# Optimization experiments

Hardware: AMD Instinct MI355X
Metric: run time of the kernel (lower is better)

The kernel has to match this reference:

```python
import jax, jax.numpy as jnp
import numpy as np

B, T, C = 2, 2048, 1024
H = 16
D = C // H
STRIDE = 2
EPS = 1e-5


def _strided_allowed(T, stride):
    # position i attends to j if j<=i and (j >= i-4 local band OR j % stride == 0)
    i = jnp.arange(T)[:, None]
    j = jnp.arange(T)[None, :]
    return (j <= i) & ((j >= i - 4) | (j % stride == 0))


def _layernorm(x, w, b):
    mu = jnp.mean(x, axis=-1, keepdims=True)
    var = jnp.mean(jnp.square(x - mu), axis=-1, keepdims=True)
    return (x - mu) * jax.lax.rsqrt(var + EPS) * w + b


def setup_inputs() -> dict:
    key = jax.random.key(0)
    ks = jax.random.split(key, 8)
    s = 0.02
    return {
        "x": jax.random.normal(ks[0], (B, T, C), dtype=jnp.float32),
        "ln1_w": jnp.ones((C,), jnp.float32),
        "ln1_b": jnp.zeros((C,), jnp.float32),
        "c_attn_w": s * jax.random.normal(ks[1], (C, 3 * C), jnp.float32),  # [in,out]
        "c_attn_b": jnp.zeros((3 * C,), jnp.float32),
        "attn_proj_w": s * jax.random.normal(ks[2], (C, C), jnp.float32),
        "attn_proj_b": jnp.zeros((C,), jnp.float32),
        "ln2_w": jnp.ones((C,), jnp.float32),
        "ln2_b": jnp.zeros((C,), jnp.float32),
        "fc_w": s * jax.random.normal(ks[3], (C, 4 * C), jnp.float32),
        "fc_b": jnp.zeros((4 * C,), jnp.float32),
        "mlp_proj_w": s * jax.random.normal(ks[4], (4 * C, C), jnp.float32),
        "mlp_proj_b": jnp.zeros((C,), jnp.float32),
    }


def reference(x, ln1_w, ln1_b, c_attn_w, c_attn_b, attn_proj_w, attn_proj_b,
              ln2_w, ln2_b, fc_w, fc_b, mlp_proj_w, mlp_proj_b):
    Bx, Tx, Cx = x.shape
    # --- sparse (strided) causal attention on ln_1(x) ---
    h = _layernorm(x, ln1_w, ln1_b)
    qkv = h @ c_attn_w + c_attn_b                      # [B,T,3C]
    q, k, v = jnp.split(qkv, 3, axis=-1)
    q = q.reshape(Bx, Tx, H, D).transpose(0, 2, 1, 3)  # [B,H,T,D]
    k = k.reshape(Bx, Tx, H, D).transpose(0, 2, 1, 3)
    v = v.reshape(Bx, Tx, H, D).transpose(0, 2, 1, 3)
    scale = 1.0 / np.sqrt(D)
    att = jnp.einsum('bhqd,bhkd->bhqk', q, k) * scale  # dense [B,H,T,T] as in source
    allowed = _strided_allowed(Tx, STRIDE)             # [T,T] bool
    att = jnp.where(allowed[None, None], att, -jnp.inf)
    att = jax.nn.softmax(att, axis=-1)
    y = jnp.einsum('bhqk,bhkd->bhqd', att, v)
    y = y.transpose(0, 2, 1, 3).reshape(Bx, Tx, Cx)
    y = y @ attn_proj_w + attn_proj_b
    x = x + y
    # --- MLP on ln_2(x) ---
    h2 = _layernorm(x, ln2_w, ln2_b)
    h2 = jax.nn.gelu(h2 @ fc_w + fc_b, approximate=False)
    x = x + (h2 @ mlp_proj_w + mlp_proj_b)
    return x
```

## Files before the change

### kernel.cpp

```cpp
#include <hip/hip_runtime.h>
#include <hip/hip_bf16.h>

#define Bn 2
#define Tn 2048
#define Cn 1024
#define Hn 16
#define Dn 64
#define Mrows (Bn * Tn)

typedef __attribute__((ext_vector_type(8))) short short8;
typedef __attribute__((ext_vector_type(4))) float f32x4;

typedef const __attribute__((address_space(1))) unsigned int* gas_ptr;
typedef __attribute__((address_space(3))) unsigned int* las_ptr;

__device__ __forceinline__ unsigned short f2b(float f) {
  unsigned int u = __builtin_bit_cast(unsigned int, f);
  return (unsigned short)((u + 0x7fffu + ((u >> 16) & 1u)) >> 16);
}

__device__ __forceinline__ float gelu_f(float v) {
  float u2 = v + 0.044715f * v * v * v;
  float e = __expf(1.5957691216f * u2);
  float th = 1.0f - 2.0f / (e + 1.0f);
  return 0.5f * v * (1.0f + th);
}

__global__ __launch_bounds__(256) void ln_kernel(const float* __restrict__ x,
                                                 const float* __restrict__ w,
                                                 const float* __restrict__ b,
                                                 unsigned short* __restrict__ out) {
  const int row = blockIdx.x;
  const int t = threadIdx.x;
  const float4 v = *reinterpret_cast<const float4*>(x + (size_t)row * Cn + t * 4);
  float s = v.x + v.y + v.z + v.w;
  float s2 = v.x * v.x + v.y * v.y + v.z * v.z + v.w * v.w;
#pragma unroll
  for (int m = 1; m < 64; m <<= 1) { s += __shfl_xor(s, m); s2 += __shfl_xor(s2, m); }
  __shared__ float ls[4], ls2[4];
  if ((t & 63) == 0) { ls[t >> 6] = s; ls2[t >> 6] = s2; }
  __syncthreads();
  s  = ls[0] + ls[1] + ls[2] + ls[3];
  s2 = ls2[0] + ls2[1] + ls2[2] + ls2[3];
  const float mu = s * (1.0f / Cn);
  const float rstd = rsqrtf(s2 * (1.0f / Cn) - mu * mu + 1e-5f);
  const float4 wv = *reinterpret_cast<const float4*>(w + t * 4);
  const float4 bv = *reinterpret_cast<const float4*>(b + t * 4);
  unsigned short o[4];
  o[0] = f2b((v.x - mu) * rstd * wv.x + bv.x);
  o[1] = f2b((v.y - mu) * rstd * wv.y + bv.y);
  o[2] = f2b((v.z - mu) * rstd * wv.z + bv.z);
  o[3] = f2b((v.w - mu) * rstd * wv.w + bv.w);
  *reinterpret_cast<uint2*>(out + (size_t)row * Cn + t * 4) = *reinterpret_cast<uint2*>(o);
}

__global__ __launch_bounds__(256) void transpose_bf16_kernel(const float* __restrict__ W,
                                                             unsigned short* __restrict__ Wt,
                                                             int K, int N) {
  __shared__ float tile[32][33];
  const int n0 = blockIdx.x * 32, k0 = blockIdx.y * 32;
  const int tx = threadIdx.x & 31, ty = threadIdx.x >> 5;
#pragma unroll
  for (int r = 0; r < 4; r++)
    tile[ty + r * 8][tx] = W[(size_t)(k0 + ty + r * 8) * N + n0 + tx];
  __syncthreads();
#pragma unroll
  for (int r = 0; r < 4; r++)
    Wt[(size_t)(n0 + ty + r * 8) * K + k0 + tx] = f2b(tile[tx][ty + r * 8]);
}

#define BUFS 16384
template <int EP>
__global__ __launch_bounds__(512, 2) void gemm256_kernel(
    const unsigned short* __restrict__ A, const unsigned short* __restrict__ Bt,
    const float* __restrict__ bias, void* out, int M, int N, int K, int nx) {
  extern __shared__ unsigned short lds[];
  const int tid = threadIdx.x;
  const int lane = tid & 63, w = tid >> 6;
  const int wm = w >> 2, wn = w & 3;
  const int l15 = lane & 15, l4 = lane >> 4;

  const int nwg = gridDim.x;
  int wg = blockIdx.x;
  wg = (wg & 7) * (nwg >> 3) + (wg >> 3);
  const int tile_m = (wg / nx) * 256;
  const int tile_n = (wg % nx) * 256;

  f32x4 acc[8][4] = {};

  const int ch0 = w * 64 + lane;
  const int r0 = ch0 >> 2;
  const int c0 = (((ch0 & 3) ^ ((r0 >> 1) & 3))) * 8;
  const unsigned short* gA0 = A + (size_t)(tile_m + r0) * K + c0;
  const unsigned short* gA1 = gA0 + (size_t)128 * K;
  const unsigned short* gB0 = Bt + (size_t)(tile_n + r0) * K + c0;
  const unsigned short* gB1 = gB0 + (size_t)128 * K;
  const int ldsA0 = (w * 64) * 8, ldsA1 = (512 + w * 64) * 8;

  auto stage = [&](unsigned short* Ab, int t) {
    unsigned short* Bb = Ab + 8192;
    const size_t ko = (size_t)t * 32;
    __builtin_amdgcn_global_load_lds((gas_ptr)(gA0 + ko), (las_ptr)&Ab[ldsA0], 16, 0, 0);
    __builtin_amdgcn_global_load_lds((gas_ptr)(gA1 + ko), (las_ptr)&Ab[ldsA1], 16, 0, 0);
    __builtin_amdgcn_global_load_lds((gas_ptr)(gB0 + ko), (las_ptr)&Bb[ldsA0], 16, 0, 0);
    __builtin_amdgcn_global_load_lds((gas_ptr)(gB1 + ko), (las_ptr)&Bb[ldsA1], 16, 0, 0);
  };

  stage(lds, 0);
  stage(lds + BUFS, 1);
  stage(lds + 2 * BUFS, 2);
  asm volatile("s_waitcnt vmcnt(8)" ::: "memory");
  __builtin_amdgcn_s_barrier();
  __builtin_amdgcn_sched_barrier(0);

  const int ca = (l4 ^ ((l15 >> 1) & 3)) * 8;

  const int nt = K >> 5;
  for (int tb = 0; tb < nt; tb += 4) {
#pragma unroll
    for (int u = 0; u < 4; u++) {
      const int t = tb + u;
      if (t + 3 < nt) stage(lds + (((u + 3) & 3) * BUFS), t + 3);

      const unsigned short* Ab = lds + u * BUFS;
      const unsigned short* Bb = Ab + 8192;
      short8 a[4], b[4], a2[4];
#pragma unroll
      for (int i = 0; i < 4; i++) {
        a[i] = *reinterpret_cast<const short8*>(&Ab[(wm * 128 + i * 16 + l15) * 32 + ca]);
        b[i] = *reinterpret_cast<const short8*>(&Bb[(wn * 64 + i * 16 + l15) * 32 + ca]);
      }
      __builtin_amdgcn_sched_barrier(0);
#pragma unroll
      for (int i = 0; i < 4; i++)
        a2[i] = *reinterpret_cast<const short8*>(&Ab[(wm * 128 + 64 + i * 16 + l15) * 32 + ca]);

      asm volatile("s_waitcnt lgkmcnt(4)" ::: "memory");
      __builtin_amdgcn_sched_barrier(0);
      __builtin_amdgcn_s_setprio(1);
#pragma unroll
      for (int mi = 0; mi < 4; mi++)
#pragma unroll
        for (int ni = 0; ni < 4; ni++)
          acc[mi][ni] = __builtin_amdgcn_mfma_f32_16x16x32_bf16(a[mi], b[ni], acc[mi][ni], 0, 0, 0);
      __builtin_amdgcn_s_setprio(0);
      __builtin_amdgcn_sched_barrier(0);

      asm volatile("s_waitcnt lgkmcnt(0)" ::: "memory");
      __builtin_amdgcn_sched_barrier(0);
      __builtin_amdgcn_s_setprio(1);
#pragma unroll
      for (int mi = 0; mi < 4; mi++)
#pragma unroll
        for (int ni = 0; ni < 4; ni++)
          acc[mi + 4][ni] = __builtin_amdgcn_mfma_f32_16x16x32_bf16(a2[mi], b[ni], acc[mi + 4][ni], 0, 0, 0);
      __builtin_amdgcn_s_setprio(0);
      __builtin_amdgcn_sched_barrier(0);

      if (t + 3 < nt) {
        asm volatile("s_waitcnt vmcnt(8)" ::: "memory");
      } else if (t + 2 < nt) {
        asm volatile("s_waitcnt vmcnt(4)" ::: "memory");
      } else if (t + 1 < nt) {
        asm volatile("s_waitcnt vmcnt(0)" ::: "memory");
      }
      __builtin_amdgcn_s_barrier();
      __builtin_amdgcn_sched_barrier(0);
    }
  }

#pragma unroll
  for (int ni = 0; ni < 4; ni++) {
    const int col = tile_n + wn * 64 + ni * 16 + l15;
    const float bv = bias[col];
#pragma unroll
    for (int mi = 0; mi < 8; mi++) {
#pragma unroll
      for (int r = 0; r < 4; r++) {
        const int row = tile_m + wm * 128 + mi * 16 + l4 * 4 + r;
        const size_t idx = (size_t)row * N + col;
        float v = acc[mi][ni][r] + bv;
        if (EP == 0) {
          ((unsigned short*)out)[idx] = f2b(v);
        } else {
          ((unsigned short*)out)[idx] = f2b(gelu_f(v));
        }
      }
    }
  }
}

__global__ __launch_bounds__(512, 2) void gemm128_kernel(
    const unsigned short* __restrict__ A, const unsigned short* __restrict__ Bt,
    const float* __restrict__ bias, const float* __restrict__ res, float* __restrict__ out,
    int M, int N, int K, int nx) {
  extern __shared__ unsigned short lds[];
  const int tid = threadIdx.x;
  const int lane = tid & 63, w = tid >> 6;
  const int wm = w >> 2, wn = w & 3;
  const int l15 = lane & 15, l4 = lane >> 4;

  const int nwg = gridDim.x;
  int wg = blockIdx.x;
  wg = (wg & 7) * (nwg >> 3) + (wg >> 3);
  const int tile_m = (wg / nx) * 128;
  const int tile_n = (wg % nx) * 128;

  f32x4 acc[4][2] = {};

  const unsigned short* Gs = (w < 4) ? A : Bt;
  const int tb0 = (w < 4) ? tile_m : tile_n;
  const int ch0 = (w & 3) * 128 + lane;
  const int r0c = ch0 >> 2;
  const int c0s = (((ch0 & 3) ^ ((r0c >> 1) & 3))) * 8;
  const unsigned short* g0 = Gs + (size_t)(tb0 + r0c) * K + c0s;
  const unsigned short* g1 = g0 + (size_t)16 * K;
  const int lds0 = ((w & 3) * 128) * 8, lds1 = ((w & 3) * 128 + 64) * 8;
  const int half = (w < 4) ? 0 : 4096;

  auto stage = [&](unsigned short* slot, int t) {
    unsigned short* Lb = slot + half;
    const size_t ko = (size_t)t * 32;
    __builtin_amdgcn_global_load_lds((gas_ptr)(g0 + ko), (las_ptr)&Lb[lds0], 16, 0, 0);
    __builtin_amdgcn_global_load_lds((gas_ptr)(g1 + ko), (las_ptr)&Lb[lds1], 16, 0, 0);
  };

  stage(lds, 0);
  stage(lds + 8192, 1);
  stage(lds + 16384, 2);
  asm volatile("s_waitcnt vmcnt(4)" ::: "memory");
  __builtin_amdgcn_s_barrier();
  __builtin_amdgcn_sched_barrier(0);

  const int ca = (l4 ^ ((l15 >> 1) & 3)) * 8;

  const int nt = K >> 5;
  for (int tb = 0; tb < nt; tb += 4) {
#pragma unroll
    for (int u = 0; u < 4; u++) {
      const int t = tb + u;
      if (t + 3 < nt) stage(lds + ((u + 3) & 3) * 8192, t + 3);

      const unsigned short* Ab = lds + u * 8192;
      const unsigned short* Bb = Ab + 4096;
      short8 a[2], b[2], a2[2];
#pragma unroll
      for (int i = 0; i < 2; i++) {
        a[i] = *reinterpret_cast<const short8*>(&Ab[(wm * 64 + i * 16 + l15) * 32 + ca]);
        b[i] = *reinterpret_cast<const short8*>(&Bb[(wn * 32 + i * 16 + l15) * 32 + ca]);
      }
      __builtin_amdgcn_sched_barrier(0);
#pragma unroll
      for (int i = 0; i < 2; i++)
        a2[i] = *reinterpret_cast<const short8*>(&Ab[(wm * 64 + 32 + i * 16 + l15) * 32 + ca]);

      asm volatile("s_waitcnt lgkmcnt(2)" ::: "memory");
      __builtin_amdgcn_sched_barrier(0);
      __builtin_amdgcn_s_setprio(1);
#pragma unroll
      for (int mi = 0; mi < 2; mi++)
#pragma unroll
        for (int ni = 0; ni < 2; ni++)
          acc[mi][ni] = __builtin_amdgcn_mfma_f32_16x16x32_bf16(a[mi], b[ni], acc[mi][ni], 0, 0, 0);
      __builtin_amdgcn_s_setprio(0);
      __builtin_amdgcn_sched_barrier(0);

      asm volatile("s_waitcnt lgkmcnt(0)" ::: "memory");
      __builtin_amdgcn_sched_barrier(0);
      __builtin_amdgcn_s_setprio(1);
#pragma unroll
      for (int mi = 0; mi < 2; mi++)
#pragma unroll
        for (int ni = 0; ni < 2; ni++)
          acc[mi + 2][ni] = __builtin_amdgcn_mfma_f32_16x16x32_bf16(a2[mi], b[ni], acc[mi + 2][ni], 0, 0, 0);
      __builtin_amdgcn_s_setprio(0);
      __builtin_amdgcn_sched_barrier(0);

      if (t + 3 < nt) {
        asm volatile("s_waitcnt vmcnt(4)" ::: "memory");
      } else if (t + 2 < nt) {
        asm volatile("s_waitcnt vmcnt(2)" ::: "memory");
      } else if (t + 1 < nt) {
        asm volatile("s_waitcnt vmcnt(0)" ::: "memory");
      }
      __builtin_amdgcn_s_barrier();
      __builtin_amdgcn_sched_barrier(0);
    }
  }

#pragma unroll
  for (int ni = 0; ni < 2; ni++) {
    const int col = tile_n + wn * 32 + ni * 16 + l15;
    const float bv = bias[col];
#pragma unroll
    for (int mi = 0; mi < 4; mi++) {
#pragma unroll
      for (int r = 0; r < 4; r++) {
        const int row = tile_m + wm * 64 + mi * 16 + l4 * 4 + r;
        const size_t idx = (size_t)row * N + col;
        out[idx] = acc[mi][ni][r] + bv + res[idx];
      }
    }
  }
}

__global__ __launch_bounds__(256, 4) void attn_kernel(const unsigned short* __restrict__ qkv,
                                                      unsigned short* __restrict__ y) {
  __shared__ unsigned short SH[17408];
  const int tid = threadIdx.x;
  const int lane = tid & 63, w = tid >> 6;
  const int l15 = lane & 15, l4 = lane >> 4;

  const int bi = blockIdx.x;
  const int quarter = bi >> 8, rest = bi & 255;
  const int bh = rest >> 3, sub = rest & 7;
  int qt;
  if (quarter == 0) qt = sub;
  else if (quarter == 1) qt = 15 - sub;
  else if (quarter == 2) qt = 16 + sub;
  else qt = 31 - sub;
  const int bb = bh >> 4, hh = bh & 15;
  const int q0 = qt * 64;
  const size_t base = (size_t)bb * Tn * (3 * Cn) + hh * 64;

  const int nfar = qt >> 1;
  const int ntiles = nfar + (q0 ? 2 : 1);

  unsigned short* Vt = SH + 8192;
  unsigned short* Ps = SH + 12800 + w * 1152;

  auto keyof = [&](int t, int row) -> int {
    if (t < nfar) return t * 128 + 2 * row;
    return q0 - 64 * (ntiles - 1 - t) + row;
  };
  auto stageK = [&](int t) {
    unsigned short* kb = SH + ((t & 1) << 12);
#pragma unroll
    for (int u = 0; u < 2; u++) {
      const int chunk = u * 256 + tid;
      const int row = chunk >> 3, cc = chunk & 7;
      const int csrc = cc ^ (row & 7);
      const int key = keyof(t, row);
      __builtin_amdgcn_global_load_lds(
          (gas_ptr)&qkv[base + Cn + (size_t)key * (3 * Cn) + csrc * 8],
          (las_ptr)&kb[(u * 256 + (w << 6)) * 8], 16, 0, 0);
    }
  };
  uint4 vr[2];
  auto fetchV = [&](int t) {
#pragma unroll
    for (int u = 0; u < 2; u++) {
      const int chunk = u * 256 + tid;
      const int row = chunk >> 3, cc = chunk & 7;
      const int key = keyof(t, row);
      vr[u] = *reinterpret_cast<const uint4*>(&qkv[base + 2 * Cn + (size_t)key * (3 * Cn) + cc * 8]);
    }
  };

#pragma unroll
  for (int u = 0; u < 2; u++) {
    const int chunk = u * 256 + tid;
    const int row = chunk >> 3, cc = chunk & 7;
    const int csrc = cc ^ (row & 7);
    __builtin_amdgcn_global_load_lds(
        (gas_ptr)&qkv[base + (size_t)(q0 + row) * (3 * Cn) + csrc * 8],
        (las_ptr)&SH[(u * 256 + (w << 6)) * 8], 16, 0, 0);
  }
  __syncthreads();
  short8 qf[2];
#pragma unroll
  for (int ks = 0; ks < 2; ks++) {
    const int r = (w << 4) + l15;
    qf[ks] = *reinterpret_cast<const short8*>(&SH[r * 64 + (((ks * 4 + l4) ^ (l15 & 7)) * 8)]);
  }
  asm volatile("s_waitcnt lgkmcnt(0)" ::: "memory");
  __builtin_amdgcn_s_barrier();
  __builtin_amdgcn_sched_barrier(0);
  stageK(0);
  fetchV(0);
  __syncthreads();

  f32x4 acc_o[4] = {};
  float mrow[4], lrow[4];
#pragma unroll
  for (int r = 0; r < 4; r++) { mrow[r] = -1e30f; lrow[r] = 0.0f; }

  for (int t = 0; t < ntiles; ++t) {
#pragma unroll
    for (int u = 0; u < 2; u++) {
      const int chunk = u * 256 + tid;
      const int row = chunk >> 3, cc = chunk & 7;
      unsigned short tmp[8];
      *reinterpret_cast<uint4*>(tmp) = vr[u];
      const int xr = row ^ (cc << 3);
#pragma unroll
      for (int j = 0; j < 8; j++) Vt[(cc * 8 + j) * 72 + xr] = tmp[j];
    }
    if (t + 1 < ntiles) { stageK(t + 1); fetchV(t + 1); }
    asm volatile("s_waitcnt lgkmcnt(0)" ::: "memory");
    __builtin_amdgcn_s_barrier();
    __builtin_amdgcn_sched_barrier(0);

    const unsigned short* Kb = SH + ((t & 1) << 12);
    f32x4 s[4] = {};
#pragma unroll
    for (int ni = 0; ni < 4; ni++) {
#pragma unroll
      for (int ks = 0; ks < 2; ks++) {
        const int r = ni * 16 + l15;
        short8 kf = *reinterpret_cast<const short8*>(&Kb[r * 64 + (((ks * 4 + l4) ^ (l15 & 7)) * 8)]);
        s[ni] = __builtin_amdgcn_mfma_f32_16x16x32_bf16(qf[ks], kf, s[ni], 0, 0, 0);
      }
    }

    const bool far = (t < nfar);
    const int kb0 = far ? t * 128 : q0 - 64 * (ntiles - 1 - t);
#pragma unroll
    for (int ni = 0; ni < 4; ni++) {
      const int pos = ni * 16 + l15;
      const int j = far ? kb0 + 2 * pos : kb0 + pos;
#pragma unroll
      for (int r = 0; r < 4; r++) {
        float v = s[ni][r] * 0.125f;
        if (far) {
          v = (j < q0 - 64) ? v : -1e30f;
        } else {
          const int iq = q0 + (w << 4) + l4 * 4 + r;
          const bool ok = (j <= iq) && ((j >= iq - 4) || ((j & 1) == 0));
          v = ok ? v : -1e30f;
        }
        s[ni][r] = v;
      }
    }

#pragma unroll
    for (int r = 0; r < 4; r++) {
      float tm = fmaxf(fmaxf(s[0][r], s[1][r]), fmaxf(s[2][r], s[3][r]));
      tm = fmaxf(tm, __shfl_xor(tm, 1));
      tm = fmaxf(tm, __shfl_xor(tm, 2));
      tm = fmaxf(tm, __shfl_xor(tm, 4));
      tm = fmaxf(tm, __shfl_xor(tm, 8));
      const float mnew = fmaxf(mrow[r], tm);
      const float alpha = __expf(mrow[r] - mnew);
      mrow[r] = mnew;
      lrow[r] *= alpha;
#pragma unroll
      for (int nd = 0; nd < 4; nd++) acc_o[nd][r] *= alpha;
      float rs = 0.0f;
#pragma unroll
      for (int ni = 0; ni < 4; ni++) {
        const float pv = __expf(s[ni][r] - mnew);
        s[ni][r] = pv;
        rs += pv;
      }
      rs += __shfl_xor(rs, 1); rs += __shfl_xor(rs, 2);
      rs += __shfl_xor(rs, 4); rs += __shfl_xor(rs, 8);
      lrow[r] += rs;
    }

#pragma unroll
    for (int ni = 0; ni < 4; ni++)
#pragma unroll
      for (int r = 0; r < 4; r++)
        Ps[(l4 * 4 + r) * 72 + ni * 16 + l15] = f2b(s[ni][r]);

#pragma unroll
    for (int kss = 0; kss < 2; kss++) {
      short8 pf = *reinterpret_cast<const short8*>(&Ps[l15 * 72 + kss * 32 + l4 * 8]);
#pragma unroll
      for (int nd = 0; nd < 4; nd++) {
        const int d = nd * 16 + l15;
        const int kcol = (kss * 32 + l4 * 8) ^ ((d >> 3) << 3);
        short8 vf = *reinterpret_cast<const short8*>(&Vt[d * 72 + kcol]);
        acc_o[nd] = __builtin_amdgcn_mfma_f32_16x16x32_bf16(pf, vf, acc_o[nd], 0, 0, 0);
      }
    }

    __syncthreads();
  }

#pragma unroll
  for (int r = 0; r < 4; r++) {
    const float inv = 1.0f / lrow[r];
    const int row = q0 + (w << 4) + l4 * 4 + r;
#pragma unroll
    for (int nd = 0; nd < 4; nd++) {
      const int col = nd * 16 + l15;
      y[((size_t)bb * Tn + row) * Cn + hh * 64 + col] = f2b(acc_o[nd][r] * inv);
    }
  }
}

extern "C" void kernel_launch(void* const* d_in, const int* in_sizes, int n_in,
                              void* d_out, int out_size, void* d_ws, size_t ws_size,
                              hipStream_t stream) {
  const float* x           = (const float*)d_in[0];
  const float* ln1_w       = (const float*)d_in[1];
  const float* ln1_b       = (const float*)d_in[2];
  const float* c_attn_w    = (const float*)d_in[3];
  const float* c_attn_b    = (const float*)d_in[4];
  const float* attn_proj_w = (const float*)d_in[5];
  const float* attn_proj_b = (const float*)d_in[6];
  const float* ln2_w       = (const float*)d_in[7];
  const float* ln2_b       = (const float*)d_in[8];
  const float* fc_w        = (const float*)d_in[9];
  const float* fc_b        = (const float*)d_in[10];
  const float* mlp_proj_w  = (const float*)d_in[11];
  const float* mlp_proj_b  = (const float*)d_in[12];
  float* out = (float*)d_out;

  char* ws = (char*)d_ws;
  unsigned short* wT1 = (unsigned short*)(ws);
  unsigned short* wT2 = (unsigned short*)(ws + 6291456);
  unsigned short* wT3 = (unsigned short*)(ws + 8388608);
  unsigned short* wT4 = (unsigned short*)(ws + 16777216);
  unsigned short* h   = (unsigned short*)(ws + 25165824);
  unsigned short* qkv = (unsigned short*)(ws + 33554432);
  unsigned short* yb  = (unsigned short*)(ws + 67108864);

  hipFuncSetAttribute((const void*)gemm256_kernel<0>, hipFuncAttributeMaxDynamicSharedMemorySize, 131072);
  hipFuncSetAttribute((const void*)gemm256_kernel<2>, hipFuncAttributeMaxDynamicSharedMemorySize, 131072);
  hipFuncSetAttribute((const void*)gemm128_kernel, hipFuncAttributeMaxDynamicSharedMemorySize, 65536);

  transpose_bf16_kernel<<<dim3(3072 / 32, 1024 / 32), 256, 0, stream>>>(c_attn_w, wT1, 1024, 3072);
  transpose_bf16_kernel<<<dim3(1024 / 32, 1024 / 32), 256, 0, stream>>>(attn_proj_w, wT2, 1024, 1024);
  transpose_bf16_kernel<<<dim3(4096 / 32, 1024 / 32), 256, 0, stream>>>(fc_w, wT3, 1024, 4096);
  transpose_bf16_kernel<<<dim3(1024 / 32, 4096 / 32), 256, 0, stream>>>(mlp_proj_w, wT4, 4096, 1024);

  ln_kernel<<<Mrows, 256, 0, stream>>>(x, ln1_w, ln1_b, h);
  gemm256_kernel<0><<<(Mrows / 256) * (3072 / 256), 512, 131072, stream>>>(
      h, wT1, c_attn_b, qkv, Mrows, 3072, 1024, 3072 / 256);
  attn_kernel<<<1024, 256, 0, stream>>>(qkv, yb);
  gemm128_kernel<<<(Mrows / 128) * (1024 / 128), 512, 65536, stream>>>(
      yb, wT2, attn_proj_b, x, out, Mrows, 1024, 1024, 1024 / 128);
  ln_kernel<<<Mrows, 256, 0, stream>>>(out, ln2_w, ln2_b, h);
  gemm256_kernel<2><<<(Mrows / 256) * (4096 / 256), 512, 131072, stream>>>(
      h, wT3, fc_b, qkv, Mrows, 4096, 1024, 4096 / 256);
  gemm128_kernel<<<(Mrows / 128) * (1024 / 128), 512, 65536, stream>>>(
      qkv, wT4, mlp_proj_b, out, out, Mrows, 1024, 4096, 1024 / 128);
}
```

Measured before the change: 228.7 us.

## Fuse weight prep with LN1, deepen gemm128 pipeline, lazily rescale softmax

Merges the four weight transpose launches and the first layernorm into one prep kernel to cut launch overhead and tail gaps. Rewrites the gemm128 main loop to process two K-steps per iteration with a six-slot LDS ring and a prefetch distance of four, raising its shared memory to 96KB and launch bounds to one block per CU. In attention, the online-softmax rescale now runs only when some row maximum grows by more than 8, skipping exp/multiply work at the cost of possibly larger unnormalized values. The lower occupancy in gemm128 may offset its deeper prefetch.

New measurement: 221.4 us. 3.2% less time.

```diff
diff --git a/kernel.cpp b/kernel.cpp
--- a/kernel.cpp
+++ b/kernel.cpp
@@ -26,18 +26,15 @@
   return 0.5f * v * (1.0f + th);
 }
 
-__global__ __launch_bounds__(256) void ln_kernel(const float* __restrict__ x,
-                                                 const float* __restrict__ w,
-                                                 const float* __restrict__ b,
-                                                 unsigned short* __restrict__ out) {
-  const int row = blockIdx.x;
+__device__ __forceinline__ void ln_row(const float* __restrict__ x, const float* __restrict__ w,
+                                       const float* __restrict__ b, unsigned short* __restrict__ out,
+                                       int row, float* ls, float* ls2) {
   const int t = threadIdx.x;
   const float4 v = *reinterpret_cast<const float4*>(x + (size_t)row * Cn + t * 4);
   float s = v.x + v.y + v.z + v.w;
   float s2 = v.x * v.x + v.y * v.y + v.z * v.z + v.w * v.w;
 #pragma unroll
   for (int m = 1; m < 64; m <<= 1) { s += __shfl_xor(s, m); s2 += __shfl_xor(s2, m); }
-  __shared__ float ls[4], ls2[4];
   if ((t & 63) == 0) { ls[t >> 6] = s; ls2[t >> 6] = s2; }
   __syncthreads();
   s  = ls[0] + ls[1] + ls[2] + ls[3];
@@ -54,11 +51,35 @@
   *reinterpret_cast<uint2*>(out + (size_t)row * Cn + t * 4) = *reinterpret_cast<uint2*>(o);
 }
 
-__global__ __launch_bounds__(256) void transpose_bf16_kernel(const float* __restrict__ W,
-                                                             unsigned short* __restrict__ Wt,
-                                                             int K, int N) {
+__global__ __launch_bounds__(256) void ln_kernel(const float* __restrict__ x,
+                                                 const float* __restrict__ w,
+                                                 const float* __restrict__ b,
+                                                 unsigned short* __restrict__ out) {
+  __shared__ float ls[4], ls2[4];
+  ln_row(x, w, b, out, blockIdx.x, ls, ls2);
+}
+
+__global__ __launch_bounds__(256) void prep_kernel(
+    const float* __restrict__ W0, unsigned short* __restrict__ T0,
+    const float* __restrict__ W1, unsigned short* __restrict__ T1,
+    const float* __restrict__ W2, unsigned short* __restrict__ T2,
+    const float* __restrict__ W3, unsigned short* __restrict__ T3,
+    const float* __restrict__ x, const float* __restrict__ ln1w,
+    const float* __restrict__ ln1b, unsigned short* __restrict__ h) {
   __shared__ float tile[32][33];
-  const int n0 = blockIdx.x * 32, k0 = blockIdx.y * 32;
+  __shared__ float ls[4], ls2[4];
+  int b = blockIdx.x;
+  if (b >= 12288) {
+    ln_row(x, ln1w, ln1b, h, b - 12288, ls, ls2);
+    return;
+  }
+  const float* W; unsigned short* T; int K, N;
+  if (b < 3072)      { W = W0; T = T0; K = 1024; N = 3072; }
+  else if (b < 4096) { W = W1; T = T1; K = 1024; N = 1024; b -= 3072; }
+  else if (b < 8192) { W = W2; T = T2; K = 1024; N = 4096; b -= 4096; }
+  else               { W = W3; T = T3; K = 4096; N = 1024; b -= 8192; }
+  const int nx = N >> 5;
+  const int n0 = (b % nx) * 32, k0 = (b / nx) * 32;
   const int tx = threadIdx.x & 31, ty = threadIdx.x >> 5;
 #pragma unroll
   for (int r = 0; r < 4; r++)
@@ -66,7 +87,7 @@
   __syncthreads();
 #pragma unroll
   for (int r = 0; r < 4; r++)
-    Wt[(size_t)(n0 + ty + r * 8) * K + k0 + tx] = f2b(tile[tx][ty + r * 8]);
+    T[(size_t)(n0 + ty + r * 8) * K + k0 + tx] = f2b(tile[tx][ty + r * 8]);
 }
 
 #define BUFS 16384
@@ -190,7 +211,7 @@
   }
 }
 
-__global__ __launch_bounds__(512, 2) void gemm128_kernel(
+__global__ __launch_bounds__(512, 1) void gemm128_kernel(
     const unsigned short* __restrict__ A, const unsigned short* __restrict__ Bt,
     const float* __restrict__ bias, const float* __restrict__ res, float* __restrict__ out,
     int M, int N, int K, int nx) {
@@ -218,16 +239,17 @@
   const int lds0 = ((w & 3) * 128) * 8, lds1 = ((w & 3) * 128 + 64) * 8;
   const int half = (w < 4) ? 0 : 4096;
 
-  auto stage = [&](unsigned short* slot, int t) {
-    unsigned short* Lb = slot + half;
+  auto stage = [&](int slot, int t) {
+    unsigned short* Lb = lds + slot * 8192 + half;
     const size_t ko = (size_t)t * 32;
     __builtin_amdgcn_global_load_lds((gas_ptr)(g0 + ko), (las_ptr)&Lb[lds0], 16, 0, 0);
     __builtin_amdgcn_global_load_lds((gas_ptr)(g1 + ko), (las_ptr)&Lb[lds1], 16, 0, 0);
   };
 
-  stage(lds, 0);
-  stage(lds + 8192, 1);
-  stage(lds + 16384, 2);
+  stage(0, 0);
+  stage(1, 1);
+  stage(2, 2);
+  stage(3, 3);
   asm volatile("s_waitcnt vmcnt(4)" ::: "memory");
   __builtin_amdgcn_s_barrier();
   __builtin_amdgcn_sched_barrier(0);
@@ -235,57 +257,88 @@
   const int ca = (l4 ^ ((l15 >> 1) & 3)) * 8;
 
   const int nt = K >> 5;
-  for (int tb = 0; tb < nt; tb += 4) {
-#pragma unroll
-    for (int u = 0; u < 4; u++) {
-      const int t = tb + u;
-      if (t + 3 < nt) stage(lds + ((u + 3) & 3) * 8192, t + 3);
-
-      const unsigned short* Ab = lds + u * 8192;
-      const unsigned short* Bb = Ab + 4096;
-      short8 a[2], b[2], a2[2];
-#pragma unroll
-      for (int i = 0; i < 2; i++) {
-        a[i] = *reinterpret_cast<const short8*>(&Ab[(wm * 64 + i * 16 + l15) * 32 + ca]);
-        b[i] = *reinterpret_cast<const short8*>(&Bb[(wn * 32 + i * 16 + l15) * 32 + ca]);
-      }
-      __builtin_amdgcn_sched_barrier(0);
-#pragma unroll
-      for (int i = 0; i < 2; i++)
-        a2[i] = *reinterpret_cast<const short8*>(&Ab[(wm * 64 + 32 + i * 16 + l15) * 32 + ca]);
-
-      asm volatile("s_waitcnt lgkmcnt(2)" ::: "memory");
-      __builtin_amdgcn_sched_barrier(0);
-      __builtin_amdgcn_s_setprio(1);
-#pragma unroll
-      for (int mi = 0; mi < 2; mi++)
-#pragma unroll
-        for (int ni = 0; ni < 2; ni++)
-          acc[mi][ni] = __builtin_amdgcn_mfma_f32_16x16x32_bf16(a[mi], b[ni], acc[mi][ni], 0, 0, 0);
-      __builtin_amdgcn_s_setprio(0);
-      __builtin_amdgcn_sched_barrier(0);
-
-      asm volatile("s_waitcnt lgkmcnt(0)" ::: "memory");
-      __builtin_amdgcn_sched_barrier(0);
-      __builtin_amdgcn_s_setprio(1);
-#pragma unroll
-      for (int mi = 0; mi < 2; mi++)
-#pragma unroll
-        for (int ni = 0; ni < 2; ni++)
-          acc[mi + 2][ni] = __builtin_amdgcn_mfma_f32_16x16x32_bf16(a2[mi], b[ni], acc[mi + 2][ni], 0, 0, 0);
-      __builtin_amdgcn_s_setprio(0);
-      __builtin_amdgcn_sched_barrier(0);
-
-      if (t + 3 < nt) {
-        asm volatile("s_waitcnt vmcnt(4)" ::: "memory");
-      } else if (t + 2 < nt) {
-        asm volatile("s_waitcnt vmcnt(2)" ::: "memory");
-      } else if (t + 1 < nt) {
-        asm volatile("s_waitcnt vmcnt(0)" ::: "memory");
-      }
-      __builtin_amdgcn_s_barrier();
-      __builtin_amdgcn_sched_barrier(0);
-    }
+  const int np = nt >> 1;
+  for (int p = 0; p < np; ++p) {
+    const int t0 = 2 * p;
+    if (t0 + 4 < nt) stage((t0 + 4) % 6, t0 + 4);
+    if (t0 + 5 < nt) stage((t0 + 5) % 6, t0 + 5);
+
+    const unsigned short* A0 = lds + (t0 % 6) * 8192;
+    const unsigned short* B0 = A0 + 4096;
+    const unsigned short* A1 = lds + ((t0 + 1) % 6) * 8192;
+    const unsigned short* B1 = A1 + 4096;
+    short8 a[2], b[2], a2[2], c[2], d[2], c2[2];
+#pragma unroll
+    for (int i = 0; i < 2; i++) {
+      a[i] = *reinterpret_cast<const short8*>(&A0[(wm * 64 + i * 16 + l15) * 32 + ca]);
+      b[i] = *reinterpret_cast<const short8*>(&B0[(wn * 32 + i * 16 + l15) * 32 + ca]);
+    }
+    __builtin_amdgcn_sched_barrier(0);
+#pragma unroll
+    for (int i = 0; i < 2; i++)
+      a2[i] = *reinterpret_cast<const short8*>(&A0[(wm * 64 + 32 + i * 16 + l15) * 32 + ca]);
+    __builtin_amdgcn_sched_barrier(0);
+#pragma unroll
+    for (int i = 0; i < 2; i++) {
+      c[i] = *reinterpret_cast<const short8*>(&A1[(wm * 64 + i * 16 + l15) * 32 + ca]);
+      d[i] = *reinterpret_cast<const short8*>(&B1[(wn * 32 + i * 16 + l15) * 32 + ca]);
+    }
+    __builtin_amdgcn_sched_barrier(0);
+#pragma unroll
+    for (int i = 0; i < 2; i++)
+      c2[i] = *reinterpret_cast<const short8*>(&A1[(wm * 64 + 32 + i * 16 + l15) * 32 + ca]);
+
+    asm volatile("s_waitcnt lgkmcnt(8)" ::: "memory");
+    __builtin_amdgcn_sched_barrier(0);
+    __builtin_amdgcn_s_setprio(1);
+#pragma unroll
+    for (int mi = 0; mi < 2; mi++)
+#pragma unroll
+      for (int ni = 0; ni < 2; ni++)
+        acc[mi][ni] = __builtin_amdgcn_mfma_f32_16x16x32_bf16(a[mi], b[ni], acc[mi][ni], 0, 0, 0);
+    __builtin_amdgcn_s_setprio(0);
+    __builtin_amdgcn_sched_barrier(0);
+
+    asm volatile("s_waitcnt lgkmcnt(6)" ::: "memory");
+    __builtin_amdgcn_sched_barrier(0);
+    __builtin_amdgcn_s_setprio(1);
+#pragma unroll
+    for (int mi = 0; mi < 2; mi++)
+#pragma unroll
+      for (int ni = 0; ni < 2; ni++)
+        acc[mi + 2][ni] = __builtin_amdgcn_mfma_f32_16x16x32_bf16(a2[mi], b[ni], acc[mi + 2][ni], 0, 0, 0);
+    __builtin_amdgcn_s_setprio(0);
+    __builtin_amdgcn_sched_barrier(0);
+
+    asm volatile("s_waitcnt lgkmcnt(2)" ::: "memory");
+    __builtin_amdgcn_sched_barrier(0);
+    __builtin_amdgcn_s_setprio(1);
+#pragma unroll
+    for (int mi = 0; mi < 2; mi++)
+#pragma unroll
+      for (int ni = 0; ni < 2; ni++)
+        acc[mi][ni] = __builtin_amdgcn_mfma_f32_16x16x32_bf16(c[mi], d[ni], acc[mi][ni], 0, 0, 0);
+    __builtin_amdgcn_s_setprio(0);
+    __builtin_amdgcn_sched_barrier(0);
+
+    asm volatile("s_waitcnt lgkmcnt(0)" ::: "memory");
+    __builtin_amdgcn_sched_barrier(0);
+    __builtin_amdgcn_s_setprio(1);
+#pragma unroll
+    for (int mi = 0; mi < 2; mi++)
+#pragma unroll
+      for (int ni = 0; ni < 2; ni++)
+        acc[mi + 2][ni] = __builtin_amdgcn_mfma_f32_16x16x32_bf16(c2[mi], d[ni], acc[mi + 2][ni], 0, 0, 0);
+    __builtin_amdgcn_s_setprio(0);
+    __builtin_amdgcn_sched_barrier(0);
+
+    if (t0 + 4 < nt) {
+      asm volatile("s_waitcnt vmcnt(4)" ::: "memory");
+    } else if (t0 + 2 < nt) {
+      asm volatile("s_waitcnt vmcnt(0)" ::: "memory");
+    }
+    __builtin_amdgcn_s_barrier();
+    __builtin_amdgcn_sched_barrier(0);
   }
 
 #pragma unroll
@@ -433,6 +486,8 @@
       }
     }
 
+    float tmx[4];
+    bool need = false;
 #pragma unroll
     for (int r = 0; r < 4; r++) {
       float tm = fmaxf(fmaxf(s[0][r], s[1][r]), fmaxf(s[2][r], s[3][r]));
@@ -440,16 +495,26 @@
       tm = fmaxf(tm, __shfl_xor(tm, 2));
       tm = fmaxf(tm, __shfl_xor(tm, 4));
       tm = fmaxf(tm, __shfl_xor(tm, 8));
-      const float mnew = fmaxf(mrow[r], tm);
-      const float alpha = __expf(mrow[r] - mnew);
-      mrow[r] = mnew;
-      lrow[r] *= alpha;
-#pragma unroll
-      for (int nd = 0; nd < 4; nd++) acc_o[nd][r] *= alpha;
+      tmx[r] = tm;
+      need = need || (tm > mrow[r] + 8.0f);
+    }
+    if (__any(need)) {
+#pragma unroll
+      for (int r = 0; r < 4; r++) {
+        const float mnew = fmaxf(mrow[r], tmx[r]);
+        const float alpha = __expf(mrow[r] - mnew);
+        mrow[r] = mnew;
+        lrow[r] *= alpha;
+#pragma unroll
+        for (int nd = 0; nd < 4; nd++) acc_o[nd][r] *= alpha;
+      }
+    }
+#pragma unroll
+    for (int r = 0; r < 4; r++) {
       float rs = 0.0f;
 #pragma unroll
       for (int ni = 0; ni < 4; ni++) {
-        const float pv = __expf(s[ni][r] - mnew);
+        const float pv = __expf(s[ni][r] - mrow[r]);
         s[ni][r] = pv;
         rs += pv;
       }
@@ -520,22 +585,19 @@
 
   hipFuncSetAttribute((const void*)gemm256_kernel<0>, hipFuncAttributeMaxDynamicSharedMemorySize, 131072);
   hipFuncSetAttribute((const void*)gemm256_kernel<2>, hipFuncAttributeMaxDynamicSharedMemorySize, 131072);
-  hipFuncSetAttribute((const void*)gemm128_kernel, hipFuncAttributeMaxDynamicSharedMemorySize, 65536);
-
-  transpose_bf16_kernel<<<dim3(3072 / 32, 1024 / 32), 256, 0, stream>>>(c_attn_w, wT1, 1024, 3072);
-  transpose_bf16_kernel<<<dim3(1024 / 32, 1024 / 32), 256, 0, stream>>>(attn_proj_w, wT2, 1024, 1024);
-  transpose_bf16_kernel<<<dim3(4096 / 32, 1024 / 32), 256, 0, stream>>>(fc_w, wT3, 1024, 4096);
-  transpose_bf16_kernel<<<dim3(1024 / 32, 4096 / 32), 256, 0, stream>>>(mlp_proj_w, wT4, 4096, 1024);
-
-  ln_kernel<<<Mrows, 256, 0, stream>>>(x, ln1_w, ln1_b, h);
+  hipFuncSetAttribute((const void*)gemm128_kernel, hipFuncAttributeMaxDynamicSharedMemorySize, 98304);
+
+  prep_kernel<<<16384, 256, 0, stream>>>(c_attn_w, wT1, attn_proj_w, wT2,
+                                         fc_w, wT3, mlp_proj_w, wT4,
+                                         x, ln1_w, ln1_b, h);
   gemm256_kernel<0><<<(Mrows / 256) * (3072 / 256), 512, 131072, stream>>>(
       h, wT1, c_attn_b, qkv, Mrows, 3072, 1024, 3072 / 256);
   attn_kernel<<<1024, 256, 0, stream>>>(qkv, yb);
-  gemm128_kernel<<<(Mrows / 128) * (1024 / 128), 512, 65536, stream>>>(
+  gemm128_kernel<<<(Mrows / 128) * (1024 / 128), 512, 98304, stream>>>(
       yb, wT2, attn_proj_b, x, out, Mrows, 1024, 1024, 1024 / 128);
   ln_kernel<<<Mrows, 256, 0, stream>>>(out, ln2_w, ln2_b, h);
   gemm256_kernel<2><<<(Mrows / 256) * (4096 / 256), 512, 131072, stream>>>(
       h, wT3, fc_b, qkv, Mrows, 4096, 1024, 4096 / 256);
-  gemm128_kernel<<<(Mrows / 128) * (1024 / 128), 512, 65536, stream>>>(
+  gemm128_kernel<<<(Mrows / 128) * (1024 / 128), 512, 98304, stream>>>(
       qkv, wT4, mlp_proj_b, out, out, Mrows, 1024, 4096, 1024 / 128);
 }
```
